# Kernel tuning notes

Hardware: AMD Instinct MI355X
Metric: run time of the kernel (lower is better)

## Reference

```python
import jax, jax.numpy as jnp
import numpy as np

RC = 5.0
N_ATYPE = 10
ACSF_NMU = 20
APSF_NMU = 10
ACSF_ETA = 100.0
APSF_ETA = 25.0
N_ATOMS = 30000
N_PAIRS = 200000
MAX_NB = 6
DENSE = 64
FEAT_DIM = ACSF_NMU * N_ATYPE + APSF_NMU * N_ATYPE + 22  # 322
ZINDEX = jnp.array([1.0, 3.0, 5.0, 6.0, 7.0, 8.0, 9.0, 11.0, 15.0, 16.0])
CHARGE_KEYS = jnp.array([0.0, 1.0, 3.0, 5.0, 6.0, 7.0, 8.0, 9.0, 11.0, 15.0, 16.0])
CHARGE_VALS = jnp.array([100000, 0, 1, 2, 3, 4, 5, 6, 7, 8, 9])


def pbc_shift(dr, box, box_inv):
    ds = dr @ box_inv
    ds = ds - jnp.floor(ds + 0.5)
    return ds @ box


def int_to_onehot(labels, num_classes):
    zidx = CHARGE_VALS[jnp.searchsorted(CHARGE_KEYS, labels)]
    return jax.nn.one_hot(zidx, num_classes, dtype=labels.dtype)


def dense_ln_relu(x, W, b, g, beta):
    h = x @ W + b
    mu = jnp.mean(h, axis=-1, keepdims=True)
    var = jnp.mean(jnp.square(h - mu), axis=-1, keepdims=True)
    return jax.nn.relu((h - mu) * jax.lax.rsqrt(var + 1e-6) * g + beta)


def forward(pos, box, valid_mask, W1, b1, g1, be1, W2, b2, g2, be2, W3, b3, g3, be3, Wo, bo,
            pairs, topo_nblist, topo_mask, mol_ID, atype_indices):
    dt = pos.dtype
    acsf_mus = jnp.linspace(0.0, 5.0, ACSF_NMU).astype(dt)
    apsf_mus = jnp.linspace(-1.0, 1.0, APSF_NMU).astype(dt)
    mScales = jnp.array([0.0, 0.0, 0.0, 0.0, 0.0, 1.0], dtype=dt)
    # regularize_pairs: padded pairs have i >= j, shift them off-diagonal
    p = pairs[:, :2]
    dp_flag = (p[:, 1] - p[:, 0] <= 0).astype(p.dtype)
    p = p - jnp.stack([dp_flag, 2 * dp_flag], axis=1)
    nbonds = pairs[:, 2]
    buffer_scales = (p[:, 0] < p[:, 1]).astype(dt) * valid_mask
    mscales = mScales[nbonds - 1] * buffer_scales  # computed as in original (unused downstream)
    box_inv = jnp.linalg.inv(box)
    ri = pos[p[:, 0]]
    rj = pos[p[:, 1]]
    rij = pbc_shift(rj - ri, box, box_inv)
    dr_norm = jnp.linalg.norm(rij + 1e-10, axis=1)
    same_mol = mol_ID[p[:, 0]] == mol_ID[p[:, 1]]
    buffer_inter = jnp.where(same_mol, 0.0, 1.0).astype(dt)
    cutoff = jnp.where(dr_norm <= RC, 0.5 * (1 + jnp.cos(jnp.pi * dr_norm / RC)), 0.0)
    buffer_nblist_inter_rc = buffer_inter * buffer_scales * cutoff
    # environment atoms of each pair endpoint (bonded topology neighbors)
    j_nb = topo_nblist[p[:, 0]]  # [P, M]
    k_nb = topo_nblist[p[:, 1]]
    j_mask = topo_mask[p[:, 0]] & (j_nb != -1) & (j_nb != p[:, 0:1]) & (j_nb != p[:, 1:2])
    k_mask = topo_mask[p[:, 1]] & (k_nb != -1) & (k_nb != p[:, 0:1]) & (k_nb != p[:, 1:2])
    rij_unit = rij / (dr_norm[:, None] + 1e-10)

    def cos_gamma(center, nb, mask, unit):
        r_env = jnp.where(mask[..., None], pos[nb], 0.0)  # [P, M, 3]
        rX = pbc_shift(r_env - center[:, None, :], box, box_inv)
        rXn = rX / jnp.linalg.norm(rX + 1e-10, axis=2, keepdims=True)
        return jnp.einsum('pmi,pi->pm', rXn, unit) * mask

    cos_gamma_i = cos_gamma(ri, j_nb, j_mask, rij_unit)
    cos_gamma_j = cos_gamma(rj, k_nb, k_mask, -rij_unit)
    type_cols = jnp.arange(N_ATYPE)

    def apsf(cg, nb, mask):
        feat = jnp.exp(-APSF_ETA * jnp.square(cg[..., None] - apsf_mus)) * mask[..., None]
        onehot = (atype_indices[nb][..., None] == type_cols).astype(dt)
        return jnp.einsum('pmk,pml->pkl', feat, onehot)  # [P, APSF_NMU, N_ATYPE]

    G_pair = (apsf(cos_gamma_i, j_nb, j_mask) + apsf(cos_gamma_j, k_nb, k_mask)) * 0.5 \
             * buffer_nblist_inter_rc[:, None, None]
    # ACSF radial atom-centered features
    r_env = pos[topo_nblist]  # [N, M, 3]
    dr = pbc_shift(r_env - pos[:, None, :], box, box_inv)
    dnorm = jnp.linalg.norm(dr + 1e-10, axis=2)
    fx = dnorm / RC
    f_cut = jnp.where(fx < 1, 0.5 * (jnp.cos(jnp.pi * fx) + 1), 0.0) * topo_mask
    G_raw = jnp.exp(-ACSF_ETA * jnp.square(dnorm[..., None] - acsf_mus)) * f_cut[..., None]
    nb_onehot = (atype_indices[topo_nblist][..., None] == type_cols).astype(dt)
    G_atom = jnp.einsum('nmk,nml->nkl', G_raw, nb_onehot)  # [N, ACSF_NMU, N_ATYPE]
    atom_feat = 0.5 * (G_atom[p[:, 0]] + G_atom[p[:, 1]])
    # element charge + one-hot block
    elem = ZINDEX[atype_indices].astype(dt)
    j_z = elem[p[:, 0]]
    k_z = elem[p[:, 1]]
    atype_onehot = jnp.concatenate([j_z[:, None], int_to_onehot(j_z, 10),
                                    k_z[:, None], int_to_onehot(k_z, 10)], axis=1)
    feats = jnp.concatenate([atom_feat.reshape(atom_feat.shape[0], -1),
                             G_pair.reshape(G_pair.shape[0], -1),
                             atype_onehot], axis=1)  # [P, 322]
    # MLP energy head
    x = dense_ln_relu(feats, W1, b1, g1, be1)
    x = dense_ln_relu(x, W2, b2, g2, be2)
    x = dense_ln_relu(x, W3, b3, g3, be3)
    out_AB = x @ Wo + bo
    return jnp.sum(out_AB * buffer_nblist_inter_rc[:, None])


def setup_inputs() -> dict:
    key = jax.random.key(0)
    ks = jax.random.split(key, 16)
    L = 30.0
    pos = jax.random.uniform(ks[0], (N_ATOMS, 3), jnp.float32, 0.0, L)
    box = jnp.eye(3, dtype=jnp.float32) * L
    i = jax.random.randint(ks[1], (N_PAIRS,), 2, N_ATOMS)
    j = jax.random.randint(ks[2], (N_PAIRS,), 2, N_ATOMS)
    p0 = jnp.minimum(i, j)
    p1 = jnp.maximum(i, j)
    pairs = jnp.stack([p0, p1, jnp.full((N_PAIRS,), 6, dtype=p0.dtype)], axis=1)
    valid_mask = (jax.random.uniform(ks[3], (N_PAIRS,)) < 0.95).astype(jnp.float32)
    nb = jax.random.randint(ks[4], (N_ATOMS, MAX_NB), 0, N_ATOMS)
    topo_nblist = jnp.where(jax.random.uniform(ks[5], (N_ATOMS, MAX_NB)) < 0.25, -1, nb)
    topo_mask = topo_nblist != -1
    mol_ID = jnp.arange(N_ATOMS, dtype=jnp.int32) // 3
    atype_indices = jax.random.randint(ks[6], (N_ATOMS,), 0, N_ATYPE)

    def dense_w(k, fin, fout):
        return jax.random.normal(k, (fin, fout), jnp.float32) / np.float32(np.sqrt(fin))

    return {
        'pos': pos, 'box': box, 'valid_mask': valid_mask,
        'W1': dense_w(ks[7], FEAT_DIM, DENSE), 'b1': jnp.zeros((DENSE,), jnp.float32),
        'g1': jnp.ones((DENSE,), jnp.float32), 'be1': jnp.zeros((DENSE,), jnp.float32),
        'W2': dense_w(ks[8], DENSE, DENSE), 'b2': jnp.zeros((DENSE,), jnp.float32),
        'g2': jnp.ones((DENSE,), jnp.float32), 'be2': jnp.zeros((DENSE,), jnp.float32),
        'W3': dense_w(ks[9], DENSE, DENSE), 'b3': jnp.zeros((DENSE,), jnp.float32),
        'g3': jnp.ones((DENSE,), jnp.float32), 'be3': jnp.zeros((DENSE,), jnp.float32),
        'Wo': dense_w(ks[10], DENSE, 1), 'bo': jnp.zeros((1,), jnp.float32),
        'pairs': pairs, 'topo_nblist': topo_nblist, 'topo_mask': topo_mask,
        'mol_ID': mol_ID, 'atype_indices': atype_indices,
    }


def reference(pos, box, valid_mask, W1, b1, g1, be1, W2, b2, g2, be2, W3, b3, g3, be3, Wo, bo,
              pairs, topo_nblist, topo_mask, mol_ID, atype_indices):
    return forward(pos, box, valid_mask, W1, b1, g1, be1, W2, b2, g2, be2, W3, b3, g3, be3, Wo, bo,
                   pairs, topo_nblist, topo_mask, mol_ID, atype_indices)
```

## Files before the change

kernel.cpp:

```cpp
#include <hip/hip_runtime.h>
#include <math.h>

#define N_PAIRS_C 200000
#define MAX_NB_C 6
#define RC_F 5.0f
#define PI_F 3.14159265358979323846f
#define NBLK 256
#define NTHR 512
#define NWAVE 8
#define SLICE 782
#define LCAP 96
#define PPW 3
#define W1S 324
#define W23S 68

__device__ __constant__ float c_ZIND[10] = {1.f, 3.f, 5.f, 6.f, 7.f, 8.f, 9.f, 11.f, 15.f, 16.f};

__device__ __forceinline__ void invert3x3(const float* b, float* inv) {
    float a00 = b[0], a01 = b[1], a02 = b[2];
    float a10 = b[3], a11 = b[4], a12 = b[5];
    float a20 = b[6], a21 = b[7], a22 = b[8];
    float det = a00 * (a11 * a22 - a12 * a21)
              - a01 * (a10 * a22 - a12 * a20)
              + a02 * (a10 * a21 - a11 * a20);
    float id = 1.0f / det;
    inv[0] =  (a11 * a22 - a12 * a21) * id;
    inv[1] = -(a01 * a22 - a02 * a21) * id;
    inv[2] =  (a01 * a12 - a02 * a11) * id;
    inv[3] = -(a10 * a22 - a12 * a20) * id;
    inv[4] =  (a00 * a22 - a02 * a20) * id;
    inv[5] = -(a00 * a12 - a02 * a10) * id;
    inv[6] =  (a10 * a21 - a11 * a20) * id;
    inv[7] = -(a00 * a21 - a01 * a20) * id;
    inv[8] =  (a00 * a11 - a01 * a10) * id;
}

__device__ __forceinline__ void pbc3(float dx, float dy, float dz,
                                     const float* box, const float* binv,
                                     float& ox, float& oy, float& oz) {
    float s0 = dx * binv[0] + dy * binv[3] + dz * binv[6];
    float s1 = dx * binv[1] + dy * binv[4] + dz * binv[7];
    float s2 = dx * binv[2] + dy * binv[5] + dz * binv[8];
    s0 -= floorf(s0 + 0.5f);
    s1 -= floorf(s1 + 0.5f);
    s2 -= floorf(s2 + 0.5f);
    ox = s0 * box[0] + s1 * box[3] + s2 * box[6];
    oy = s0 * box[1] + s1 * box[4] + s2 * box[7];
    oz = s0 * box[2] + s1 * box[5] + s2 * box[8];
}

__device__ __forceinline__ float wsum64(float v) {
    #pragma unroll
    for (int off = 32; off > 0; off >>= 1) v += __shfl_xor(v, off, 64);
    return v;
}

__device__ __forceinline__ float ln_relu(float h, float g, float be) {
    float mu = wsum64(h) * 0.015625f;
    float d  = h - mu;
    float var = wsum64(d * d) * 0.015625f;
    float r = d * (1.0f / sqrtf(var + 1e-6f)) * g + be;
    return fmaxf(r, 0.0f);
}

__device__ __forceinline__ float rlf(float v, int lane) {
    return __int_as_float(__builtin_amdgcn_readlane(__float_as_int(v), lane));
}
__device__ __forceinline__ int rli(int v, int lane) {
    return __builtin_amdgcn_readlane(v, lane);
}

__global__ __launch_bounds__(NTHR) void fused_kernel(
    const float* __restrict__ pos,
    const float* __restrict__ box,
    const float* __restrict__ valid_mask,
    const float* __restrict__ W1, const float* __restrict__ b1,
    const float* __restrict__ g1, const float* __restrict__ be1,
    const float* __restrict__ W2, const float* __restrict__ b2,
    const float* __restrict__ g2, const float* __restrict__ be2,
    const float* __restrict__ W3, const float* __restrict__ b3,
    const float* __restrict__ g3, const float* __restrict__ be3,
    const float* __restrict__ Wo, const float* __restrict__ bo,
    const int* __restrict__ pairs,
    const int* __restrict__ nblist,
    const int* __restrict__ atype,
    const int* __restrict__ mol_ID,
    float* __restrict__ out) {

    __shared__ __align__(16) float W1t[64][W1S];
    __shared__ __align__(16) float W2t[64][W23S];
    __shared__ __align__(16) float W3t[64][W23S];
    __shared__ int   l_p0[LCAP], l_p1[LCAP];
    __shared__ float l_fac[LCAP];
    __shared__ int   l_cnt;
    __shared__ float wacc[NWAVE];

    const int tid = threadIdx.x;
    const int w = tid >> 6;
    const int j = tid & 63;

    if (tid == 0) l_cnt = 0;

    float bx[9], bi[9];
    #pragma unroll
    for (int i = 0; i < 9; ++i) bx[i] = box[i];
    invert3x3(bx, bi);

    for (int q = w; q < 81; q += NWAVE) {
        int f0 = 4 * q;
        float4 v;
        v.x = W1[(f0 + 0) * 64 + j];
        v.y = W1[(f0 + 1) * 64 + j];
        v.z = (f0 + 2 < 322) ? W1[(f0 + 2) * 64 + j] : 0.0f;
        v.w = (f0 + 3 < 322) ? W1[(f0 + 3) * 64 + j] : 0.0f;
        *(float4*)&W1t[j][f0] = v;
    }
    for (int q = w; q < 16; q += NWAVE) {
        int f0 = 4 * q;
        float4 v2, v3;
        v2.x = W2[(f0 + 0) * 64 + j]; v3.x = W3[(f0 + 0) * 64 + j];
        v2.y = W2[(f0 + 1) * 64 + j]; v3.y = W3[(f0 + 1) * 64 + j];
        v2.z = W2[(f0 + 2) * 64 + j]; v3.z = W3[(f0 + 2) * 64 + j];
        v2.w = W2[(f0 + 3) * 64 + j]; v3.w = W3[(f0 + 3) * 64 + j];
        *(float4*)&W2t[j][f0] = v2;
        *(float4*)&W3t[j][f0] = v3;
    }
    __syncthreads();

    {
        int tb = blockIdx.x * SLICE;
        int lim = tb + SLICE;
        if (lim > N_PAIRS_C) lim = N_PAIRS_C;
        for (int t = tb + tid; t < lim; t += NTHR) {
            int i0 = pairs[3 * t], i1 = pairs[3 * t + 1];
            int dp = (i1 - i0 <= 0) ? 1 : 0;
            int p0 = i0 - dp, p1 = i1 - 2 * dp;
            if (p0 >= p1) continue;
            float vm = valid_mask[t];
            if (vm == 0.0f) continue;
            if (mol_ID[p0] == mol_ID[p1]) continue;
            float dx, dy, dz;
            pbc3(pos[3 * p1] - pos[3 * p0],
                 pos[3 * p1 + 1] - pos[3 * p0 + 1],
                 pos[3 * p1 + 2] - pos[3 * p0 + 2], bx, bi, dx, dy, dz);
            float ax = dx + 1e-10f, ay = dy + 1e-10f, az = dz + 1e-10f;
            float dn = sqrtf(ax * ax + ay * ay + az * az);
            if (dn > RC_F) continue;
            float fac = vm * 0.5f * (1.0f + __cosf(PI_F * dn / RC_F));
            int slot = atomicAdd(&l_cnt, 1);
            if (slot < LCAP) { l_p0[slot] = p0; l_p1[slot] = p1; l_fac[slot] = fac; }
        }
    }
    __syncthreads();

    int cnt = l_cnt;
    if (cnt > LCAP) cnt = LCAP;

    float mu_[5];
    int ty_[5], selr_[5];
    #pragma unroll
    for (int r = 0; r < 5; ++r) {
        int F = j + 64 * r;
        if (F < 200)      { mu_[r] = 5.0f * (float)(F / 10) / 19.0f; ty_[r] = F % 10; selr_[r] = 1; }
        else if (F < 300) { int G = F - 200; mu_[r] = -1.0f + 2.0f * (float)(G / 10) / 9.0f; ty_[r] = G % 10; selr_[r] = 0; }
        else              { mu_[r] = 0.0f; ty_[r] = 255; selr_[r] = 0; }
    }

    const float b1j = b1[j], g1j = g1[j], be1j = be1[j];
    const float b2j = b2[j], g2j = g2[j], be2j = be2[j];
    const float b3j = b3[j], g3j = g3[j], be3j = be3[j];
    const float woj = Wo[j], bo0 = bo[0];

    float acc = 0.0f;

    for (int base = 0; base < cnt; base += NWAVE * PPW) {
        int i0 = base + PPW * w;
        if (i0 >= cnt) break;
        int iB = i0 + 1, iC = i0 + 2;
        bool okB = iB < cnt, okC = iC < cnt;
        int p0A = l_p0[i0], p1A = l_p1[i0]; float facA = l_fac[i0];
        int p0B = okB ? l_p0[iB] : p0A, p1B = okB ? l_p1[iB] : p1A;
        float facB = okB ? l_fac[iB] : 0.0f;
        int p0C = okC ? l_p0[iC] : p0A, p1C = okC ? l_p1[iC] : p1A;
        float facC = okC ? l_fac[iC] : 0.0f;

        int tiA = atype[p0A], tjA = atype[p1A];
        int tiB = atype[p0B], tjB = atype[p1B];
        int tiC = atype[p0C], tjC = atype[p1C];

        float sdn = 1.0f, sfce = 0.0f, scg = 0.0f, sapw = 0.0f;
        int sty = 0;
        {
            bool isA = (j < 12);
            bool isB = (j >= 16 && j < 28);
            bool isC = (j >= 32 && j < 44);
            if (isA || isB || isC) {
                int s  = isA ? j : (isB ? (j - 16) : (j - 32));
                int p0 = isA ? p0A : (isB ? p0B : p0C);
                int p1 = isA ? p1A : (isB ? p1B : p1C);
                float fac = isA ? facA : (isB ? facB : facC);
                float rix = pos[3 * p0], riy = pos[3 * p0 + 1], riz = pos[3 * p0 + 2];
                float rjx = pos[3 * p1], rjy = pos[3 * p1 + 1], rjz = pos[3 * p1 + 2];
                float dxr, dyr, dzr;
                pbc3(rjx - rix, rjy - riy, rjz - riz, bx, bi, dxr, dyr, dzr);
                float axr = dxr + 1e-10f, ayr = dyr + 1e-10f, azr = dzr + 1e-10f;
                float dn0 = sqrtf(axr * axr + ayr * ayr + azr * azr);
                float idn = 1.0f / (dn0 + 1e-10f);
                float ux = dxr * idn, uy = dyr * idn, uz = dzr * idn;
                int side = (s >= 6) ? 1 : 0;
                int m = side ? (s - 6) : s;
                int a = side ? p1 : p0;
                int nb = nblist[a * MAX_NB_C + m];
                if (nb != -1) {
                    float cx = side ? rjx : rix;
                    float cy = side ? rjy : riy;
                    float cz = side ? rjz : riz;
                    float ex, ey, ez;
                    pbc3(pos[3 * nb] - cx, pos[3 * nb + 1] - cy, pos[3 * nb + 2] - cz,
                         bx, bi, ex, ey, ez);
                    float nx = ex + 1e-10f, ny = ey + 1e-10f, nz = ez + 1e-10f;
                    float dn = sqrtf(nx * nx + ny * ny + nz * nz);
                    float fr2 = dn * (1.0f / RC_F);
                    float fc = (fr2 < 1.0f) ? 0.5f * (__cosf(PI_F * fr2) + 1.0f) : 0.0f;
                    sdn = dn;
                    sfce = 0.5f * fc;
                    sty = atype[nb];
                    int pv = (nb != p0 && nb != p1) ? 1 : 0;
                    float sgn = side ? -1.0f : 1.0f;
                    scg = sgn * (ex * ux + ey * uy + ez * uz) / dn;
                    sapw = pv ? 0.5f * fac : 0.0f;
                }
            }
        }

        float frA[6] = {0.f, 0.f, 0.f, 0.f, 0.f, 0.f};
        float frB[6] = {0.f, 0.f, 0.f, 0.f, 0.f, 0.f};
        float frC[6] = {0.f, 0.f, 0.f, 0.f, 0.f, 0.f};
        #pragma unroll
        for (int s = 0; s < 12; ++s) {
            #pragma unroll
            for (int pp = 0; pp < 3; ++pp) {
                const int LB = 16 * pp;
                float dn = rlf(sdn, LB + s), fce = rlf(sfce, LB + s);
                float cg = rlf(scg, LB + s), apw = rlf(sapw, LB + s);
                int ty = rli(sty, LB + s);
                float* fr = (pp == 0) ? frA : (pp == 1) ? frB : frC;
                #pragma unroll
                for (int r = 0; r < 5; ++r) {
                    float x  = selr_[r] ? dn : cg;
                    float wg = selr_[r] ? fce : apw;
                    float td = x - mu_[r];
                    float e  = selr_[r] ? -100.0f : -25.0f;
                    fr[r] += ((ty == ty_[r]) ? wg : 0.0f) * __expf(e * td * td);
                }
            }
        }
        if (j >= 44) {
            int oh = j - 44;
            float vA, vB, vC;
            if (oh == 0)       { vA = c_ZIND[tiA]; vB = c_ZIND[tiB]; vC = c_ZIND[tiC]; }
            else if (oh <= 10) { vA = (tiA == oh - 1) ? 1.f : 0.f; vB = (tiB == oh - 1) ? 1.f : 0.f; vC = (tiC == oh - 1) ? 1.f : 0.f; }
            else if (oh == 11) { vA = c_ZIND[tjA]; vB = c_ZIND[tjB]; vC = c_ZIND[tjC]; }
            else               { vA = (tjA == oh - 12) ? 1.f : 0.f; vB = (tjB == oh - 12) ? 1.f : 0.f; vC = (tjC == oh - 12) ? 1.f : 0.f; }
            frA[4] = vA; frB[4] = vB; frC[4] = vC;
        }
        if (j == 0) { frA[5] = (tjA == 8) ? 1.f : 0.f; frB[5] = (tjB == 8) ? 1.f : 0.f; frC[5] = (tjC == 8) ? 1.f : 0.f; }
        if (j == 1) { frA[5] = (tjA == 9) ? 1.f : 0.f; frB[5] = (tjB == 9) ? 1.f : 0.f; frC[5] = (tjC == 9) ? 1.f : 0.f; }

        float hA = b1j, hB = b1j, hC = b1j;
        #pragma unroll
        for (int r = 0; r < 5; ++r) {
            #pragma unroll
            for (int gg = 0; gg < 16; ++gg) {
                float4 wv = *(const float4*)&W1t[j][64 * r + 4 * gg];
                int l0 = 4 * gg;
                hA = fmaf(rlf(frA[r], l0 + 0), wv.x, hA);
                hA = fmaf(rlf(frA[r], l0 + 1), wv.y, hA);
                hA = fmaf(rlf(frA[r], l0 + 2), wv.z, hA);
                hA = fmaf(rlf(frA[r], l0 + 3), wv.w, hA);
                hB = fmaf(rlf(frB[r], l0 + 0), wv.x, hB);
                hB = fmaf(rlf(frB[r], l0 + 1), wv.y, hB);
                hB = fmaf(rlf(frB[r], l0 + 2), wv.z, hB);
                hB = fmaf(rlf(frB[r], l0 + 3), wv.w, hB);
                hC = fmaf(rlf(frC[r], l0 + 0), wv.x, hC);
                hC = fmaf(rlf(frC[r], l0 + 1), wv.y, hC);
                hC = fmaf(rlf(frC[r], l0 + 2), wv.z, hC);
                hC = fmaf(rlf(frC[r], l0 + 3), wv.w, hC);
            }
        }
        {
            float w320 = W1t[j][320], w321 = W1t[j][321];
            hA = fmaf(rlf(frA[5], 0), w320, hA); hA = fmaf(rlf(frA[5], 1), w321, hA);
            hB = fmaf(rlf(frB[5], 0), w320, hB); hB = fmaf(rlf(frB[5], 1), w321, hB);
            hC = fmaf(rlf(frC[5], 0), w320, hC); hC = fmaf(rlf(frC[5], 1), w321, hC);
        }
        float x1A = ln_relu(hA, g1j, be1j);
        float x1B = ln_relu(hB, g1j, be1j);
        float x1C = ln_relu(hC, g1j, be1j);

        float h2A = b2j, h2B = b2j, h2C = b2j;
        #pragma unroll
        for (int gg = 0; gg < 16; ++gg) {
            float4 wv = *(const float4*)&W2t[j][4 * gg];
            int l0 = 4 * gg;
            h2A = fmaf(rlf(x1A, l0 + 0), wv.x, h2A);
            h2A = fmaf(rlf(x1A, l0 + 1), wv.y, h2A);
            h2A = fmaf(rlf(x1A, l0 + 2), wv.z, h2A);
            h2A = fmaf(rlf(x1A, l0 + 3), wv.w, h2A);
            h2B = fmaf(rlf(x1B, l0 + 0), wv.x, h2B);
            h2B = fmaf(rlf(x1B, l0 + 1), wv.y, h2B);
            h2B = fmaf(rlf(x1B, l0 + 2), wv.z, h2B);
            h2B = fmaf(rlf(x1B, l0 + 3), wv.w, h2B);
            h2C = fmaf(rlf(x1C, l0 + 0), wv.x, h2C);
            h2C = fmaf(rlf(x1C, l0 + 1), wv.y, h2C);
            h2C = fmaf(rlf(x1C, l0 + 2), wv.z, h2C);
            h2C = fmaf(rlf(x1C, l0 + 3), wv.w, h2C);
        }
        float x2A = ln_relu(h2A, g2j, be2j);
        float x2B = ln_relu(h2B, g2j, be2j);
        float x2C = ln_relu(h2C, g2j, be2j);

        float h3A = b3j, h3B = b3j, h3C = b3j;
        #pragma unroll
        for (int gg = 0; gg < 16; ++gg) {
            float4 wv = *(const float4*)&W3t[j][4 * gg];
            int l0 = 4 * gg;
            h3A = fmaf(rlf(x2A, l0 + 0), wv.x, h3A);
            h3A = fmaf(rlf(x2A, l0 + 1), wv.y, h3A);
            h3A = fmaf(rlf(x2A, l0 + 2), wv.z, h3A);
            h3A = fmaf(rlf(x2A, l0 + 3), wv.w, h3A);
            h3B = fmaf(rlf(x2B, l0 + 0), wv.x, h3B);
            h3B = fmaf(rlf(x2B, l0 + 1), wv.y, h3B);
            h3B = fmaf(rlf(x2B, l0 + 2), wv.z, h3B);
            h3B = fmaf(rlf(x2B, l0 + 3), wv.w, h3B);
            h3C = fmaf(rlf(x2C, l0 + 0), wv.x, h3C);
            h3C = fmaf(rlf(x2C, l0 + 1), wv.y, h3C);
            h3C = fmaf(rlf(x2C, l0 + 2), wv.z, h3C);
            h3C = fmaf(rlf(x2C, l0 + 3), wv.w, h3C);
        }
        float x3A = ln_relu(h3A, g3j, be3j);
        float x3B = ln_relu(h3B, g3j, be3j);
        float x3C = ln_relu(h3C, g3j, be3j);

        float rA = wsum64(x3A * woj);
        float rB = wsum64(x3B * woj);
        float rC = wsum64(x3C * woj);
        if (j == 0)
            acc += (rA + bo0) * facA + (rB + bo0) * facB + (rC + bo0) * facC;
    }

    if (j == 0) wacc[w] = acc;
    __syncthreads();
    if (tid == 0) {
        float tot = 0.0f;
        #pragma unroll
        for (int i = 0; i < NWAVE; ++i) tot += wacc[i];
        atomicAdd(out, tot);
    }
}

extern "C" void kernel_launch(void* const* d_in, const int* in_sizes, int n_in,
                              void* d_out, int out_size, void* d_ws, size_t ws_size,
                              hipStream_t stream) {
    const float* pos        = (const float*)d_in[0];
    const float* box        = (const float*)d_in[1];
    const float* valid_mask = (const float*)d_in[2];
    const float* W1  = (const float*)d_in[3];
    const float* b1  = (const float*)d_in[4];
    const float* g1  = (const float*)d_in[5];
    const float* be1 = (const float*)d_in[6];
    const float* W2  = (const float*)d_in[7];
    const float* b2  = (const float*)d_in[8];
    const float* g2  = (const float*)d_in[9];
    const float* be2 = (const float*)d_in[10];
    const float* W3  = (const float*)d_in[11];
    const float* b3  = (const float*)d_in[12];
    const float* g3  = (const float*)d_in[13];
    const float* be3 = (const float*)d_in[14];
    const float* Wo  = (const float*)d_in[15];
    const float* bo  = (const float*)d_in[16];
    const int* pairs = (const int*)d_in[17];
    const int* nbl   = (const int*)d_in[18];
    const int* mol   = (const int*)d_in[20];
    const int* aty   = (const int*)d_in[21];

    float* out = (float*)d_out;

    (void)hipMemsetAsync(out, 0, sizeof(float), stream);
    fused_kernel<<<NBLK, NTHR, 0, stream>>>(
        pos, box, valid_mask,
        W1, b1, g1, be1, W2, b2, g2, be2, W3, b3, g3, be3, Wo, bo,
        pairs, nbl, aty, mol, out);
}
```

Before: 46.01 us.

## Process two pairs per wave with XOR-swizzled shared weight rows

Each wave now runs the MLP on two pairs per iteration instead of three, which cuts live registers and code size. Loops are partially unrolled instead of fully unrolled for the same reason. The transposed weight tiles in shared memory get an XOR swizzle on their float4 column index, so lanes that read the same logical column hit different LDS banks. The trade-off is less per-wave work to hide latency and some extra index arithmetic on every weight load.

```diff
diff --git a/kernel.cpp b/kernel.cpp
--- a/kernel.cpp
+++ b/kernel.cpp
@@ -10,7 +10,6 @@
 #define NWAVE 8
 #define SLICE 782
 #define LCAP 96
-#define PPW 3
 #define W1S 324
 #define W23S 68
 
@@ -98,6 +97,7 @@
     const int tid = threadIdx.x;
     const int w = tid >> 6;
     const int j = tid & 63;
+    const int a8 = (j >> 3) & 7;
 
     if (tid == 0) l_cnt = 0;
 
@@ -107,23 +107,25 @@
     invert3x3(bx, bi);
 
     for (int q = w; q < 81; q += NWAVE) {
+        int qs = (q < 80) ? ((q & ~7) | ((q ^ a8) & 7)) : 80;
         int f0 = 4 * q;
         float4 v;
         v.x = W1[(f0 + 0) * 64 + j];
         v.y = W1[(f0 + 1) * 64 + j];
         v.z = (f0 + 2 < 322) ? W1[(f0 + 2) * 64 + j] : 0.0f;
         v.w = (f0 + 3 < 322) ? W1[(f0 + 3) * 64 + j] : 0.0f;
-        *(float4*)&W1t[j][f0] = v;
+        *(float4*)&W1t[j][4 * qs] = v;
     }
     for (int q = w; q < 16; q += NWAVE) {
+        int qs = (q & 8) | ((q ^ a8) & 7);
         int f0 = 4 * q;
         float4 v2, v3;
         v2.x = W2[(f0 + 0) * 64 + j]; v3.x = W3[(f0 + 0) * 64 + j];
         v2.y = W2[(f0 + 1) * 64 + j]; v3.y = W3[(f0 + 1) * 64 + j];
         v2.z = W2[(f0 + 2) * 64 + j]; v3.z = W3[(f0 + 2) * 64 + j];
         v2.w = W2[(f0 + 3) * 64 + j]; v3.w = W3[(f0 + 3) * 64 + j];
-        *(float4*)&W2t[j][f0] = v2;
-        *(float4*)&W3t[j][f0] = v3;
+        *(float4*)&W2t[j][4 * qs] = v2;
+        *(float4*)&W3t[j][4 * qs] = v3;
     }
     __syncthreads();
 
@@ -171,34 +173,35 @@
     const float b3j = b3[j], g3j = g3[j], be3j = be3[j];
     const float woj = Wo[j], bo0 = bo[0];
 
+    const float* w1row = &W1t[j][0];
+    const float* w2row = &W2t[j][0];
+    const float* w3row = &W3t[j][0];
+
     float acc = 0.0f;
 
-    for (int base = 0; base < cnt; base += NWAVE * PPW) {
-        int i0 = base + PPW * w;
-        if (i0 >= cnt) break;
-        int iB = i0 + 1, iC = i0 + 2;
-        bool okB = iB < cnt, okC = iC < cnt;
-        int p0A = l_p0[i0], p1A = l_p1[i0]; float facA = l_fac[i0];
+    #pragma unroll 1
+    for (int base = 0; base < cnt; base += 2 * NWAVE) {
+        int iA = base + 2 * w;
+        if (iA >= cnt) break;
+        int iB = iA + 1;
+        bool okB = iB < cnt;
+        int p0A = l_p0[iA], p1A = l_p1[iA]; float facA = l_fac[iA];
         int p0B = okB ? l_p0[iB] : p0A, p1B = okB ? l_p1[iB] : p1A;
         float facB = okB ? l_fac[iB] : 0.0f;
-        int p0C = okC ? l_p0[iC] : p0A, p1C = okC ? l_p1[iC] : p1A;
-        float facC = okC ? l_fac[iC] : 0.0f;
 
         int tiA = atype[p0A], tjA = atype[p1A];
         int tiB = atype[p0B], tjB = atype[p1B];
-        int tiC = atype[p0C], tjC = atype[p1C];
 
         float sdn = 1.0f, sfce = 0.0f, scg = 0.0f, sapw = 0.0f;
         int sty = 0;
         {
             bool isA = (j < 12);
             bool isB = (j >= 16 && j < 28);
-            bool isC = (j >= 32 && j < 44);
-            if (isA || isB || isC) {
-                int s  = isA ? j : (isB ? (j - 16) : (j - 32));
-                int p0 = isA ? p0A : (isB ? p0B : p0C);
-                int p1 = isA ? p1A : (isB ? p1B : p1C);
-                float fac = isA ? facA : (isB ? facB : facC);
+            if (isA || isB) {
+                int s  = isA ? j : (j - 16);
+                int p0 = isA ? p0A : p0B;
+                int p1 = isA ? p1A : p1B;
+                float fac = isA ? facA : facB;
                 float rix = pos[3 * p0], riy = pos[3 * p0 + 1], riz = pos[3 * p0 + 2];
                 float rjx = pos[3 * p1], rjy = pos[3 * p1 + 1], rjz = pos[3 * p1 + 2];
                 float dxr, dyr, dzr;
@@ -235,118 +238,106 @@
 
         float frA[6] = {0.f, 0.f, 0.f, 0.f, 0.f, 0.f};
         float frB[6] = {0.f, 0.f, 0.f, 0.f, 0.f, 0.f};
-        float frC[6] = {0.f, 0.f, 0.f, 0.f, 0.f, 0.f};
-        #pragma unroll
+        #pragma unroll 1
         for (int s = 0; s < 12; ++s) {
+            float dnA = rlf(sdn, s),      feA = rlf(sfce, s);
+            float cgA = rlf(scg, s),      awA = rlf(sapw, s);
+            float dnB = rlf(sdn, 16 + s), feB = rlf(sfce, 16 + s);
+            float cgB = rlf(scg, 16 + s), awB = rlf(sapw, 16 + s);
+            int tA = rli(sty, s), tB = rli(sty, 16 + s);
             #pragma unroll
-            for (int pp = 0; pp < 3; ++pp) {
-                const int LB = 16 * pp;
-                float dn = rlf(sdn, LB + s), fce = rlf(sfce, LB + s);
-                float cg = rlf(scg, LB + s), apw = rlf(sapw, LB + s);
-                int ty = rli(sty, LB + s);
-                float* fr = (pp == 0) ? frA : (pp == 1) ? frB : frC;
-                #pragma unroll
-                for (int r = 0; r < 5; ++r) {
-                    float x  = selr_[r] ? dn : cg;
-                    float wg = selr_[r] ? fce : apw;
-                    float td = x - mu_[r];
-                    float e  = selr_[r] ? -100.0f : -25.0f;
-                    fr[r] += ((ty == ty_[r]) ? wg : 0.0f) * __expf(e * td * td);
+            for (int r = 0; r < 5; ++r) {
+                float e = selr_[r] ? -100.0f : -25.0f;
+                {
+                    float x = selr_[r] ? dnA : cgA, wg = selr_[r] ? feA : awA, td = x - mu_[r];
+                    frA[r] += ((tA == ty_[r]) ? wg : 0.0f) * __expf(e * td * td);
+                }
+                {
+                    float x = selr_[r] ? dnB : cgB, wg = selr_[r] ? feB : awB, td = x - mu_[r];
+                    frB[r] += ((tB == ty_[r]) ? wg : 0.0f) * __expf(e * td * td);
                 }
             }
         }
         if (j >= 44) {
             int oh = j - 44;
-            float vA, vB, vC;
-            if (oh == 0)       { vA = c_ZIND[tiA]; vB = c_ZIND[tiB]; vC = c_ZIND[tiC]; }
-            else if (oh <= 10) { vA = (tiA == oh - 1) ? 1.f : 0.f; vB = (tiB == oh - 1) ? 1.f : 0.f; vC = (tiC == oh - 1) ? 1.f : 0.f; }
-            else if (oh == 11) { vA = c_ZIND[tjA]; vB = c_ZIND[tjB]; vC = c_ZIND[tjC]; }
-            else               { vA = (tjA == oh - 12) ? 1.f : 0.f; vB = (tjB == oh - 12) ? 1.f : 0.f; vC = (tjC == oh - 12) ? 1.f : 0.f; }
-            frA[4] = vA; frB[4] = vB; frC[4] = vC;
-        }
-        if (j == 0) { frA[5] = (tjA == 8) ? 1.f : 0.f; frB[5] = (tjB == 8) ? 1.f : 0.f; frC[5] = (tjC == 8) ? 1.f : 0.f; }
-        if (j == 1) { frA[5] = (tjA == 9) ? 1.f : 0.f; frB[5] = (tjB == 9) ? 1.f : 0.f; frC[5] = (tjC == 9) ? 1.f : 0.f; }
-
-        float hA = b1j, hB = b1j, hC = b1j;
+            float vA, vB;
+            if (oh == 0)       { vA = c_ZIND[tiA]; vB = c_ZIND[tiB]; }
+            else if (oh <= 10) { vA = (tiA == oh - 1) ? 1.f : 0.f; vB = (tiB == oh - 1) ? 1.f : 0.f; }
+            else if (oh == 11) { vA = c_ZIND[tjA]; vB = c_ZIND[tjB]; }
+            else               { vA = (tjA == oh - 12) ? 1.f : 0.f; vB = (tjB == oh - 12) ? 1.f : 0.f; }
+            frA[4] = vA; frB[4] = vB;
+        }
+        if (j == 0) { frA[5] = (tjA == 8) ? 1.f : 0.f; frB[5] = (tjB == 8) ? 1.f : 0.f; }
+        if (j == 1) { frA[5] = (tjA == 9) ? 1.f : 0.f; frB[5] = (tjB == 9) ? 1.f : 0.f; }
+
+        float hA = b1j, hB = b1j;
         #pragma unroll
         for (int r = 0; r < 5; ++r) {
-            #pragma unroll
+            #pragma unroll 2
             for (int gg = 0; gg < 16; ++gg) {
-                float4 wv = *(const float4*)&W1t[j][64 * r + 4 * gg];
+                int sgg = (gg & 8) | ((gg ^ a8) & 7);
+                float4 wv = ((const float4*)(w1row + 4 * sgg))[16 * r];
                 int l0 = 4 * gg;
-                hA = fmaf(rlf(frA[r], l0 + 0), wv.x, hA);
-                hA = fmaf(rlf(frA[r], l0 + 1), wv.y, hA);
-                hA = fmaf(rlf(frA[r], l0 + 2), wv.z, hA);
-                hA = fmaf(rlf(frA[r], l0 + 3), wv.w, hA);
-                hB = fmaf(rlf(frB[r], l0 + 0), wv.x, hB);
-                hB = fmaf(rlf(frB[r], l0 + 1), wv.y, hB);
-                hB = fmaf(rlf(frB[r], l0 + 2), wv.z, hB);
-                hB = fmaf(rlf(frB[r], l0 + 3), wv.w, hB);
-                hC = fmaf(rlf(frC[r], l0 + 0), wv.x, hC);
-                hC = fmaf(rlf(frC[r], l0 + 1), wv.y, hC);
-                hC = fmaf(rlf(frC[r], l0 + 2), wv.z, hC);
-                hC = fmaf(rlf(frC[r], l0 + 3), wv.w, hC);
+                float sA0 = rlf(frA[r], l0 + 0), sA1 = rlf(frA[r], l0 + 1);
+                float sA2 = rlf(frA[r], l0 + 2), sA3 = rlf(frA[r], l0 + 3);
+                float sB0 = rlf(frB[r], l0 + 0), sB1 = rlf(frB[r], l0 + 1);
+                float sB2 = rlf(frB[r], l0 + 2), sB3 = rlf(frB[r], l0 + 3);
+                hA = fmaf(sA0, wv.x, hA); hB = fmaf(sB0, wv.x, hB);
+                hA = fmaf(sA1, wv.y, hA); hB = fmaf(sB1, wv.y, hB);
+                hA = fmaf(sA2, wv.z, hA); hB = fmaf(sB2, wv.z, hB);
+                hA = fmaf(sA3, wv.w, hA); hB = fmaf(sB3, wv.w, hB);
             }
         }
         {
-            float w320 = W1t[j][320], w321 = W1t[j][321];
-            hA = fmaf(rlf(frA[5], 0), w320, hA); hA = fmaf(rlf(frA[5], 1), w321, hA);
-            hB = fmaf(rlf(frB[5], 0), w320, hB); hB = fmaf(rlf(frB[5], 1), w321, hB);
-            hC = fmaf(rlf(frC[5], 0), w320, hC); hC = fmaf(rlf(frC[5], 1), w321, hC);
+            float w320 = w1row[320], w321 = w1row[321];
+            float tA0 = rlf(frA[5], 0), tA1 = rlf(frA[5], 1);
+            float tB0 = rlf(frB[5], 0), tB1 = rlf(frB[5], 1);
+            hA = fmaf(tA0, w320, hA); hA = fmaf(tA1, w321, hA);
+            hB = fmaf(tB0, w320, hB); hB = fmaf(tB1, w321, hB);
         }
         float x1A = ln_relu(hA, g1j, be1j);
         float x1B = ln_relu(hB, g1j, be1j);
-        float x1C = ln_relu(hC, g1j, be1j);
-
-        float h2A = b2j, h2B = b2j, h2C = b2j;
-        #pragma unroll
+
+        float h2A = b2j, h2B = b2j;
+        #pragma unroll 2
         for (int gg = 0; gg < 16; ++gg) {
-            float4 wv = *(const float4*)&W2t[j][4 * gg];
+            int sgg = (gg & 8) | ((gg ^ a8) & 7);
+            float4 wv = ((const float4*)(w2row + 4 * sgg))[0];
             int l0 = 4 * gg;
-            h2A = fmaf(rlf(x1A, l0 + 0), wv.x, h2A);
-            h2A = fmaf(rlf(x1A, l0 + 1), wv.y, h2A);
-            h2A = fmaf(rlf(x1A, l0 + 2), wv.z, h2A);
-            h2A = fmaf(rlf(x1A, l0 + 3), wv.w, h2A);
-            h2B = fmaf(rlf(x1B, l0 + 0), wv.x, h2B);
-            h2B = fmaf(rlf(x1B, l0 + 1), wv.y, h2B);
-            h2B = fmaf(rlf(x1B, l0 + 2), wv.z, h2B);
-            h2B = fmaf(rlf(x1B, l0 + 3), wv.w, h2B);
-            h2C = fmaf(rlf(x1C, l0 + 0), wv.x, h2C);
-            h2C = fmaf(rlf(x1C, l0 + 1), wv.y, h2C);
-            h2C = fmaf(rlf(x1C, l0 + 2), wv.z, h2C);
-            h2C = fmaf(rlf(x1C, l0 + 3), wv.w, h2C);
+            float sA0 = rlf(x1A, l0 + 0), sA1 = rlf(x1A, l0 + 1);
+            float sA2 = rlf(x1A, l0 + 2), sA3 = rlf(x1A, l0 + 3);
+            float sB0 = rlf(x1B, l0 + 0), sB1 = rlf(x1B, l0 + 1);
+            float sB2 = rlf(x1B, l0 + 2), sB3 = rlf(x1B, l0 + 3);
+            h2A = fmaf(sA0, wv.x, h2A); h2B = fmaf(sB0, wv.x, h2B);
+            h2A = fmaf(sA1, wv.y, h2A); h2B = fmaf(sB1, wv.y, h2B);
+            h2A = fmaf(sA2, wv.z, h2A); h2B = fmaf(sB2, wv.z, h2B);
+            h2A = fmaf(sA3, wv.w, h2A); h2B = fmaf(sB3, wv.w, h2B);
         }
         float x2A = ln_relu(h2A, g2j, be2j);
         float x2B = ln_relu(h2B, g2j, be2j);
-        float x2C = ln_relu(h2C, g2j, be2j);
-
-        float h3A = b3j, h3B = b3j, h3C = b3j;
-        #pragma unroll
+
+        float h3A = b3j, h3B = b3j;
+        #pragma unroll 2
         for (int gg = 0; gg < 16; ++gg) {
-            float4 wv = *(const float4*)&W3t[j][4 * gg];
+            int sgg = (gg & 8) | ((gg ^ a8) & 7);
+            float4 wv = ((const float4*)(w3row + 4 * sgg))[0];
             int l0 = 4 * gg;
-            h3A = fmaf(rlf(x2A, l0 + 0), wv.x, h3A);
-            h3A = fmaf(rlf(x2A, l0 + 1), wv.y, h3A);
-            h3A = fmaf(rlf(x2A, l0 + 2), wv.z, h3A);
-            h3A = fmaf(rlf(x2A, l0 + 3), wv.w, h3A);
-            h3B = fmaf(rlf(x2B, l0 + 0), wv.x, h3B);
-            h3B = fmaf(rlf(x2B, l0 + 1), wv.y, h3B);
-            h3B = fmaf(rlf(x2B, l0 + 2), wv.z, h3B);
-            h3B = fmaf(rlf(x2B, l0 + 3), wv.w, h3B);
-            h3C = fmaf(rlf(x2C, l0 + 0), wv.x, h3C);
-            h3C = fmaf(rlf(x2C, l0 + 1), wv.y, h3C);
-            h3C = fmaf(rlf(x2C, l0 + 2), wv.z, h3C);
-            h3C = fmaf(rlf(x2C, l0 + 3), wv.w, h3C);
+            float sA0 = rlf(x2A, l0 + 0), sA1 = rlf(x2A, l0 + 1);
+            float sA2 = rlf(x2A, l0 + 2), sA3 = rlf(x2A, l0 + 3);
+            float sB0 = rlf(x2B, l0 + 0), sB1 = rlf(x2B, l0 + 1);
+            float sB2 = rlf(x2B, l0 + 2), sB3 = rlf(x2B, l0 + 3);
+            h3A = fmaf(sA0, wv.x, h3A); h3B = fmaf(sB0, wv.x, h3B);
+            h3A = fmaf(sA1, wv.y, h3A); h3B = fmaf(sB1, wv.y, h3B);
+            h3A = fmaf(sA2, wv.z, h3A); h3B = fmaf(sB2, wv.z, h3B);
+            h3A = fmaf(sA3, wv.w, h3A); h3B = fmaf(sB3, wv.w, h3B);
         }
         float x3A = ln_relu(h3A, g3j, be3j);
         float x3B = ln_relu(h3B, g3j, be3j);
-        float x3C = ln_relu(h3C, g3j, be3j);
 
         float rA = wsum64(x3A * woj);
         float rB = wsum64(x3B * woj);
-        float rC = wsum64(x3C * woj);
         if (j == 0)
-            acc += (rA + bo0) * facA + (rB + bo0) * facB + (rC + bo0) * facC;
+            acc += (rA + bo0) * facA + (rB + bo0) * facB;
     }
 
     if (j == 0) wacc[w] = acc;
```

New measurement: 47.36 us. +2.9%, slower.
